# Kernel tuning notes

Hardware: AMD Instinct MI355X
Metric: run time of the kernel (lower is better)

The kernel has to match this reference:

```python
import jax, jax.numpy as jnp
import numpy as np

B, S, D = 4, 2048, 1024
H, K = 16, 64  # n_heads, dim_k (dim_v == dim_k due to __init__ bug)


def setup_inputs() -> dict:
    key = jax.random.key(0)
    ks = jax.random.split(key, 7)
    query = jax.random.normal(ks[0], (B, S, D), dtype=jnp.float32)
    k_in = jax.random.normal(ks[1], (B, S, D), dtype=jnp.float32)
    v_in = jax.random.normal(ks[2], (B, S, D), dtype=jnp.float32)
    scale = 0.02
    Wq = jax.random.normal(ks[3], (H, D, K), dtype=jnp.float32) * scale
    Wk = jax.random.normal(ks[4], (H, D, K), dtype=jnp.float32) * scale
    Wv = jax.random.normal(ks[5], (H, D, K), dtype=jnp.float32) * scale
    Wo = jax.random.normal(ks[6], (H * K, D), dtype=jnp.float32) * scale
    return {"query": query, "key": k_in, "value": v_in,
            "Wq": Wq, "Wk": Wk, "Wv": Wv, "Wo": Wo}


def reference(query, key, value, Wq, Wk, Wv, Wo):
    # Per-head projections, batched over heads: [B,H,S,K]
    q = jnp.einsum('bsd,hdk->bhsk', query, Wq)
    k = jnp.einsum('bsd,hdk->bhsk', key, Wk)
    v = jnp.einsum('bsd,hdk->bhsk', value, Wv)
    scale = jnp.sqrt(jnp.asarray(q.shape[-1], q.dtype))
    scores = jnp.einsum('bhqk,bhmk->bhqm', q, k) / scale  # [B,H,S,S]
    attn = jax.nn.softmax(scores, axis=-1)
    out = jnp.einsum('bhqm,bhmk->bhqk', attn, v)          # [B,H,S,K]
    # Concatenate heads along feature axis: [B,S,H*K]
    concat = out.transpose(0, 2, 1, 3).reshape(out.shape[0], out.shape[2], -1)
    return concat @ Wo  # [B,S,D]
```

## Files before the change

kernel.cpp:

```cpp
#include <hip/hip_runtime.h>


typedef __bf16 bf16;
typedef __bf16 bf16x4 __attribute__((ext_vector_type(4)));
typedef __bf16 bf16x8 __attribute__((ext_vector_type(8)));
typedef float f32x4 __attribute__((ext_vector_type(4)));

#define DEV static __device__ __forceinline__

constexpr int S = 2048;
constexpr int M = 8192;
constexpr int N = 1024;
constexpr int KD = 1024;

constexpr size_t PROJ_BYTES = (size_t)M * N * 2;
constexpr size_t OFF_Q  = 0;
constexpr size_t OFF_K  = PROJ_BYTES;
constexpr size_t OFF_VT = 2 * PROJ_BYTES;
constexpr size_t OFF_AO = 3 * PROJ_BYTES;
constexpr size_t OFF_WQ = 4 * PROJ_BYTES;
constexpr size_t WB     = (size_t)KD * N * 2;
constexpr size_t OFF_WK = OFF_WQ + WB;
constexpr size_t OFF_WV = OFF_WQ + 2 * WB;
constexpr size_t OFF_WO = OFF_WQ + 3 * WB;

DEV f32x4 mfma16(bf16x8 a, bf16x8 b, f32x4 c) {
  return __builtin_amdgcn_mfma_f32_16x16x32_bf16(a, b, c, 0, 0, 0);
}

DEV void gload16(const void* g, void* l) {
  __builtin_amdgcn_global_load_lds(
      (const __attribute__((address_space(1))) void*)g,
      (__attribute__((address_space(3))) void*)l, 16, 0, 0);
}

DEV void cvt16(const float* sp, char* ldsrow, int jx0, int jx1) {
  float4 v0 = *(const float4*)(sp);
  float4 v1 = *(const float4*)(sp + 4);
  float4 v2 = *(const float4*)(sp + 8);
  float4 v3 = *(const float4*)(sp + 12);
  bf16x8 q0, q1;
  q0[0] = (bf16)v0.x; q0[1] = (bf16)v0.y; q0[2] = (bf16)v0.z; q0[3] = (bf16)v0.w;
  q0[4] = (bf16)v1.x; q0[5] = (bf16)v1.y; q0[6] = (bf16)v1.z; q0[7] = (bf16)v1.w;
  q1[0] = (bf16)v2.x; q1[1] = (bf16)v2.y; q1[2] = (bf16)v2.z; q1[3] = (bf16)v2.w;
  q1[4] = (bf16)v3.x; q1[5] = (bf16)v3.y; q1[6] = (bf16)v3.z; q1[7] = (bf16)v3.w;
  *(bf16x8*)(ldsrow + jx0 * 16) = q0;
  *(bf16x8*)(ldsrow + jx1 * 16) = q1;
}

__global__ __launch_bounds__(256) void prep_weights(
    const float* __restrict__ Wq, const float* __restrict__ Wk,
    const float* __restrict__ Wv, const float* __restrict__ Wo,
    bf16* __restrict__ Wqt, bf16* __restrict__ Wkt,
    bf16* __restrict__ Wvt, bf16* __restrict__ Wot) {
  __shared__ bf16 T[64][72];
  const int t = threadIdx.x;
  const int wsel = blockIdx.x >> 8;
  const int tile = blockIdx.x & 255;
  const int ti = tile >> 4, tj = tile & 15;
  const int r = t >> 2, c16 = (t & 3) * 16;

  const float* src;
  if (wsel < 3) {
    const float* W = (wsel == 0) ? Wq : (wsel == 1) ? Wk : Wv;
    src = W + (size_t)ti * 65536 + (size_t)(tj * 64 + r) * 64 + c16;
  } else {
    src = Wo + (size_t)(tj * 64 + r) * 1024 + ti * 64 + c16;
  }
#pragma unroll
  for (int i = 0; i < 16; i += 4) {
    float4 v = *(const float4*)(src + i);
    T[r][c16 + i + 0] = (bf16)v.x;
    T[r][c16 + i + 1] = (bf16)v.y;
    T[r][c16 + i + 2] = (bf16)v.z;
    T[r][c16 + i + 3] = (bf16)v.w;
  }
  __syncthreads();
  bf16x8 o0, o1;
#pragma unroll
  for (int i = 0; i < 8; ++i) o0[i] = T[c16 + i][r];
#pragma unroll
  for (int i = 0; i < 8; ++i) o1[i] = T[c16 + 8 + i][r];
  bf16* dst;
  if (wsel < 3) {
    bf16* O = (wsel == 0) ? Wqt : (wsel == 1) ? Wkt : Wvt;
    dst = O + (size_t)(ti * 64 + r) * 1024 + tj * 64 + c16;
  } else {
    dst = Wot + (size_t)(ti * 64 + r) * 1024 + tj * 64 + c16;
  }
  *(bf16x8*)(dst) = o0;
  *(bf16x8*)(dst + 8) = o1;
}

template <int AF32, int BF32, int OMODE>
__global__ __launch_bounds__(256) void gemm_k(const void* __restrict__ Aptr,
                                              const void* __restrict__ Bptr,
                                              void* __restrict__ Outp) {
  __shared__ bf16 Al[128 * 32];
  __shared__ bf16 Bl[128 * 32];
  const int t = threadIdx.x;
  const int lane = t & 63, wid = t >> 6;
  const int g = lane >> 4, c = lane & 15;
  const int wr = wid >> 1, wc = wid & 1;
  int bx, by;
  if constexpr (OMODE == 1) { bx = blockIdx.x & 63; by = blockIdx.x >> 6; }
  else                      { by = blockIdx.x & 63; bx = blockIdx.x >> 6; }
  const int m0 = by * 128, n0 = bx * 128;

  const int p0 = t, p1 = t + 256;
  const int r0 = p0 >> 2, j0 = (p0 & 3) ^ (r0 & 3);
  const int r1 = p1 >> 2, j1 = (p1 & 3) ^ (r1 & 3);
  char* adst0 = (char*)Al + (size_t)(wid * 64) * 16;
  char* adst1 = (char*)Al + (size_t)(256 + wid * 64) * 16;
  char* bdst0 = (char*)Bl + (size_t)(wid * 64) * 16;
  char* bdst1 = (char*)Bl + (size_t)(256 + wid * 64) * 16;
  const int mS = t >> 1, hS = t & 1;
  const int jS0 = (hS * 2 + 0) ^ (mS & 3);
  const int jS1 = (hS * 2 + 1) ^ (mS & 3);

  const float* Af = (const float*)Aptr;
  const bf16*  Ab = (const bf16*)Aptr;
  const float* Bf = (const float*)Bptr;
  const bf16*  Bb = (const bf16*)Bptr;

  f32x4 acc[4][4];
#pragma unroll
  for (int i = 0; i < 4; ++i)
#pragma unroll
    for (int j = 0; j < 4; ++j) acc[i][j] = f32x4{0.f, 0.f, 0.f, 0.f};

  for (int kt = 0; kt < KD / 32; ++kt) {
    const int k0 = kt * 32;
    if constexpr (AF32) {
      cvt16(Af + (size_t)(m0 + mS) * KD + hS * 16 + k0, (char*)Al + mS * 64,
            jS0, jS1);
    } else {
      gload16(Ab + (size_t)(m0 + r0) * KD + j0 * 8 + k0, adst0);
      gload16(Ab + (size_t)(m0 + r1) * KD + j1 * 8 + k0, adst1);
    }
    if constexpr (BF32) {
      cvt16(Bf + (size_t)(n0 + mS) * KD + hS * 16 + k0, (char*)Bl + mS * 64,
            jS0, jS1);
    } else {
      gload16(Bb + (size_t)(n0 + r0) * KD + j0 * 8 + k0, bdst0);
      gload16(Bb + (size_t)(n0 + r1) * KD + j1 * 8 + k0, bdst1);
    }
    __syncthreads();
    bf16x8 af[4], bfv[4];
#pragma unroll
    for (int mi = 0; mi < 4; ++mi) {
      const int m = wr * 64 + mi * 16 + c;
      af[mi] = *(const bf16x8*)((const char*)Al + m * 64 + ((g ^ (m & 3)) * 16));
    }
#pragma unroll
    for (int ni = 0; ni < 4; ++ni) {
      const int n = wc * 64 + ni * 16 + c;
      bfv[ni] = *(const bf16x8*)((const char*)Bl + n * 64 + ((g ^ (n & 3)) * 16));
    }
#pragma unroll
    for (int mi = 0; mi < 4; ++mi)
#pragma unroll
      for (int ni = 0; ni < 4; ++ni)
        acc[mi][ni] = mfma16(af[mi], bfv[ni], acc[mi][ni]);
    __syncthreads();
  }

#pragma unroll
  for (int mi = 0; mi < 4; ++mi) {
#pragma unroll
    for (int ni = 0; ni < 4; ++ni) {
#pragma unroll
      for (int r = 0; r < 4; ++r) {
        const int m = m0 + wr * 64 + mi * 16 + 4 * g + r;
        const int n = n0 + wc * 64 + ni * 16 + c;
        const float v = acc[mi][ni][r];
        if constexpr (OMODE == 2) {
          ((float*)Outp)[(size_t)m * N + n] = v;
        } else if constexpr (OMODE == 0) {
          const int b = m >> 11, s = m & 2047, h = n >> 6, kk = n & 63;
          ((bf16*)Outp)[((size_t)(b * 16 + h) * 2048 + s) * 64 + kk] = (bf16)v;
        } else {
          const int h = m >> 6, kk = m & 63, b = n >> 11, s = n & 2047;
          ((bf16*)Outp)[((size_t)(b * 16 + h) * 64 + kk) * 2048 + s] = (bf16)v;
        }
      }
    }
  }
}

__global__ __launch_bounds__(256) void attn_k(const bf16* __restrict__ Q,
                                              const bf16* __restrict__ Kg,
                                              const bf16* __restrict__ Vg,
                                              bf16* __restrict__ AO) {
  __shared__ bf16 KT[64 * 64];
  __shared__ bf16 VTl[64 * 64];
  __shared__ bf16 P[4][16][40];
  const int t = threadIdx.x, lane = t & 63, w = t >> 6;
  const int g = lane >> 4, c = lane & 15;
  const int bh = blockIdx.x & 63, qblk = blockIdx.x >> 6;
  const int q0 = qblk * 128 + w * 32;
  const bf16* qp = Q + (size_t)bh * S * 64;
  const bf16* kp = Kg + (size_t)bh * S * 64;
  const bf16* vp = Vg + (size_t)bh * 64 * S;

  bf16x8 qf[2][2];
#pragma unroll
  for (int qt = 0; qt < 2; ++qt)
#pragma unroll
    for (int dh = 0; dh < 2; ++dh)
      qf[qt][dh] =
          *(const bf16x8*)(qp + (size_t)(q0 + qt * 16 + c) * 64 + dh * 32 + g * 8);

  int srow[4], sj[4];
#pragma unroll
  for (int k2 = 0; k2 < 4; ++k2) {
    const int pr = (t + 256 * k2) & 511;
    srow[k2] = pr >> 3;
    sj[k2] = (pr & 7) ^ (srow[k2] & 7);
  }
  bf16* dst0 = KT + (size_t)(w * 64) * 8;
  bf16* dst1 = KT + (size_t)(256 + w * 64) * 8;
  bf16* dst2 = VTl + (size_t)(w * 64) * 8;
  bf16* dst3 = VTl + (size_t)(256 + w * 64) * 8;

  f32x4 ao[2][4];
#pragma unroll
  for (int i = 0; i < 2; ++i)
#pragma unroll
    for (int j = 0; j < 4; ++j) ao[i][j] = f32x4{0.f, 0.f, 0.f, 0.f};
  float mr[2] = {0.f, 0.f};
  float lr[2] = {0.f, 0.f};
  constexpr float SC = 0.18033688011112042f;

  for (int kv0 = 0; kv0 < S; kv0 += 64) {
    gload16(kp + (size_t)(kv0 + srow[0]) * 64 + sj[0] * 8, dst0);
    gload16(kp + (size_t)(kv0 + srow[1]) * 64 + sj[1] * 8, dst1);
    gload16(vp + (size_t)srow[2] * 2048 + kv0 + sj[2] * 8, dst2);
    gload16(vp + (size_t)srow[3] * 2048 + kv0 + sj[3] * 8, dst3);
    __syncthreads();

    f32x4 st[2][4];
#pragma unroll
    for (int i = 0; i < 2; ++i)
#pragma unroll
      for (int j = 0; j < 4; ++j) st[i][j] = f32x4{0.f, 0.f, 0.f, 0.f};
#pragma unroll
    for (int dh = 0; dh < 2; ++dh) {
      bf16x8 kf[4];
#pragma unroll
      for (int sub = 0; sub < 4; ++sub) {
        const int row = sub * 16 + c;
        const int ch = (dh * 4 + g) ^ (row & 7);
        kf[sub] = *(const bf16x8*)(KT + row * 64 + ch * 8);
      }
      __builtin_amdgcn_s_setprio(1);
#pragma unroll
      for (int sub = 0; sub < 4; ++sub) {
        st[0][sub] = mfma16(kf[sub], qf[0][dh], st[0][sub]);
        st[1][sub] = mfma16(kf[sub], qf[1][dh], st[1][sub]);
      }
      __builtin_amdgcn_s_setprio(0);
    }
    bf16x8 vf[4][2];
#pragma unroll
    for (int dt = 0; dt < 4; ++dt) {
      const int row = dt * 16 + c;
#pragma unroll
      for (int s2 = 0; s2 < 2; ++s2) {
        const int ch = (s2 * 4 + g) ^ (row & 7);
        vf[dt][s2] = *(const bf16x8*)(VTl + row * 64 + ch * 8);
      }
    }
#pragma unroll
    for (int qt = 0; qt < 2; ++qt) {
      float rm = st[qt][0][0];
#pragma unroll
      for (int sub = 0; sub < 4; ++sub)
#pragma unroll
        for (int r = 0; r < 4; ++r) rm = fmaxf(rm, st[qt][sub][r]);
      rm = fmaxf(rm, __shfl_xor(rm, 16));
      rm = fmaxf(rm, __shfl_xor(rm, 32));
      const float pm = rm * SC;
      if (!__all(pm - mr[qt] <= 8.0f)) {
        const float mn = fmaxf(mr[qt], pm);
        const float corr = __builtin_amdgcn_exp2f(mr[qt] - mn);
        mr[qt] = mn;
        lr[qt] *= corr;
        float cor[4];
#pragma unroll
        for (int r = 0; r < 4; ++r)
          cor[r] = __shfl(corr, (lane & 48) + 4 * g + r);
#pragma unroll
        for (int dt = 0; dt < 4; ++dt)
#pragma unroll
          for (int r = 0; r < 4; ++r) ao[qt][dt][r] *= cor[r];
      }
      float p[16];
      float sum = 0.f;
#pragma unroll
      for (int sub = 0; sub < 4; ++sub)
#pragma unroll
        for (int r = 0; r < 4; ++r) {
          const float e = __builtin_amdgcn_exp2f(
              __builtin_fmaf(st[qt][sub][r], SC, -mr[qt]));
          p[sub * 4 + r] = e;
          sum += e;
        }
      sum += __shfl_xor(sum, 16);
      sum += __shfl_xor(sum, 32);
      lr[qt] += sum;
#pragma unroll
      for (int hh = 0; hh < 2; ++hh) {
#pragma unroll
        for (int sw = 0; sw < 2; ++sw) {
          bf16x4 t4;
#pragma unroll
          for (int r = 0; r < 4; ++r) t4[r] = (bf16)p[(2 * hh + sw) * 4 + r];
          *(bf16x4*)(&P[w][c][sw * 16 + 4 * g]) = t4;
        }
        const bf16x8 pa = *(const bf16x8*)(&P[w][c][g * 8]);
        __builtin_amdgcn_s_setprio(1);
#pragma unroll
        for (int dt = 0; dt < 4; ++dt)
          ao[qt][dt] = mfma16(pa, vf[dt][hh], ao[qt][dt]);
        __builtin_amdgcn_s_setprio(0);
      }
    }
    __syncthreads();
  }

  const int b = bh >> 4, h = bh & 15;
#pragma unroll
  for (int qt = 0; qt < 2; ++qt) {
    const float iv = 1.0f / lr[qt];
    float linv[4];
#pragma unroll
    for (int r = 0; r < 4; ++r) linv[r] = __shfl(iv, (lane & 48) + 4 * g + r);
#pragma unroll
    for (int dt = 0; dt < 4; ++dt)
#pragma unroll
      for (int r = 0; r < 4; ++r) {
        const int srow = q0 + qt * 16 + 4 * g + r;
        AO[((size_t)(b * 2048 + srow)) * 1024 + h * 64 + dt * 16 + c] =
            (bf16)(ao[qt][dt][r] * linv[r]);
      }
  }
}

extern "C" void kernel_launch(void* const* d_in, const int* in_sizes, int n_in,
                              void* d_out, int out_size, void* d_ws,
                              size_t ws_size, hipStream_t stream) {
  (void)in_sizes; (void)n_in; (void)out_size; (void)ws_size;
  const float* query = (const float*)d_in[0];
  const float* key   = (const float*)d_in[1];
  const float* value = (const float*)d_in[2];
  const float* Wq    = (const float*)d_in[3];
  const float* Wk    = (const float*)d_in[4];
  const float* Wv    = (const float*)d_in[5];
  const float* Wo    = (const float*)d_in[6];

  char* ws = (char*)d_ws;
  bf16* qb  = (bf16*)(ws + OFF_Q);
  bf16* kb  = (bf16*)(ws + OFF_K);
  bf16* vtb = (bf16*)(ws + OFF_VT);
  bf16* aob = (bf16*)(ws + OFF_AO);
  bf16* wqt = (bf16*)(ws + OFF_WQ);
  bf16* wkt = (bf16*)(ws + OFF_WK);
  bf16* wvt = (bf16*)(ws + OFF_WV);
  bf16* wot = (bf16*)(ws + OFF_WO);

  prep_weights<<<1024, 256, 0, stream>>>(Wq, Wk, Wv, Wo, wqt, wkt, wvt, wot);
  gemm_k<1, 0, 0><<<512, 256, 0, stream>>>(query, wqt, qb);
  gemm_k<1, 0, 0><<<512, 256, 0, stream>>>(key, wkt, kb);
  gemm_k<0, 1, 1><<<512, 256, 0, stream>>>(wvt, value, vtb);
  attn_k<<<1024, 256, 0, stream>>>(qb, kb, vtb, aob);
  gemm_k<0, 0, 2><<<512, 256, 0, stream>>>(aob, wot, (float*)d_out);
}
```

Measured before the change: 417.8 us.

## Double-buffer GEMM and attention LDS, pre-convert inputs, enlarge attention query tile

Input activations are now converted from fp32 to bf16 in a separate elementwise kernel, so every GEMM streams bf16 through async global-to-LDS loads. Both the GEMM and the attention kernel double-buffer their LDS tiles, prefetching the next K-step while computing the current one and removing one barrier per iteration. The attention kernel processes 64 query rows per wave instead of 32, halving the grid and reusing each K/V tile across more queries, and it writes the full 64-wide P tile at once. The costs are three extra conversion passes over the inputs, higher register pressure in attention, and doubled shared memory.

```diff
diff --git a/kernel.cpp b/kernel.cpp
--- a/kernel.cpp
+++ b/kernel.cpp
@@ -13,12 +13,12 @@
 constexpr int N = 1024;
 constexpr int KD = 1024;
 
-constexpr size_t PROJ_BYTES = (size_t)M * N * 2;
-constexpr size_t OFF_Q  = 0;
-constexpr size_t OFF_K  = PROJ_BYTES;
-constexpr size_t OFF_VT = 2 * PROJ_BYTES;
-constexpr size_t OFF_AO = 3 * PROJ_BYTES;
-constexpr size_t OFF_WQ = 4 * PROJ_BYTES;
+constexpr size_t RGN = (size_t)M * N * 2;
+constexpr size_t OFF_QB = 0;
+constexpr size_t OFF_KB = RGN;
+constexpr size_t OFF_VT = 2 * RGN;
+constexpr size_t OFF_XB = 3 * RGN;
+constexpr size_t OFF_WQ = 4 * RGN;
 constexpr size_t WB     = (size_t)KD * N * 2;
 constexpr size_t OFF_WK = OFF_WQ + WB;
 constexpr size_t OFF_WV = OFF_WQ + 2 * WB;
@@ -34,18 +34,18 @@
       (__attribute__((address_space(3))) void*)l, 16, 0, 0);
 }
 
-DEV void cvt16(const float* sp, char* ldsrow, int jx0, int jx1) {
-  float4 v0 = *(const float4*)(sp);
-  float4 v1 = *(const float4*)(sp + 4);
-  float4 v2 = *(const float4*)(sp + 8);
-  float4 v3 = *(const float4*)(sp + 12);
-  bf16x8 q0, q1;
-  q0[0] = (bf16)v0.x; q0[1] = (bf16)v0.y; q0[2] = (bf16)v0.z; q0[3] = (bf16)v0.w;
-  q0[4] = (bf16)v1.x; q0[5] = (bf16)v1.y; q0[6] = (bf16)v1.z; q0[7] = (bf16)v1.w;
-  q1[0] = (bf16)v2.x; q1[1] = (bf16)v2.y; q1[2] = (bf16)v2.z; q1[3] = (bf16)v2.w;
-  q1[4] = (bf16)v3.x; q1[5] = (bf16)v3.y; q1[6] = (bf16)v3.z; q1[7] = (bf16)v3.w;
-  *(bf16x8*)(ldsrow + jx0 * 16) = q0;
-  *(bf16x8*)(ldsrow + jx1 * 16) = q1;
+__global__ __launch_bounds__(256) void prep_in(const float* __restrict__ X,
+                                               bf16* __restrict__ Y) {
+  const int i0 = blockIdx.x * 256 + threadIdx.x;
+  const int stride = gridDim.x * 256;
+  for (int i = i0; i < (1 << 20); i += stride) {
+    float4 a = ((const float4*)X)[2 * i];
+    float4 b = ((const float4*)X)[2 * i + 1];
+    bf16x8 o;
+    o[0] = (bf16)a.x; o[1] = (bf16)a.y; o[2] = (bf16)a.z; o[3] = (bf16)a.w;
+    o[4] = (bf16)b.x; o[5] = (bf16)b.y; o[6] = (bf16)b.z; o[7] = (bf16)b.w;
+    ((bf16x8*)Y)[i] = o;
+  }
 }
 
 __global__ __launch_bounds__(256) void prep_weights(
@@ -92,12 +92,12 @@
   *(bf16x8*)(dst + 8) = o1;
 }
 
-template <int AF32, int BF32, int OMODE>
-__global__ __launch_bounds__(256) void gemm_k(const void* __restrict__ Aptr,
-                                              const void* __restrict__ Bptr,
+template <int OMODE>
+__global__ __launch_bounds__(256) void gemm_k(const bf16* __restrict__ A,
+                                              const bf16* __restrict__ Bt,
                                               void* __restrict__ Outp) {
-  __shared__ bf16 Al[128 * 32];
-  __shared__ bf16 Bl[128 * 32];
+  __shared__ bf16 Al[2][128 * 32];
+  __shared__ bf16 Bl[2][128 * 32];
   const int t = threadIdx.x;
   const int lane = t & 63, wid = t >> 6;
   const int g = lane >> 4, c = lane & 15;
@@ -110,18 +110,10 @@
   const int p0 = t, p1 = t + 256;
   const int r0 = p0 >> 2, j0 = (p0 & 3) ^ (r0 & 3);
   const int r1 = p1 >> 2, j1 = (p1 & 3) ^ (r1 & 3);
-  char* adst0 = (char*)Al + (size_t)(wid * 64) * 16;
-  char* adst1 = (char*)Al + (size_t)(256 + wid * 64) * 16;
-  char* bdst0 = (char*)Bl + (size_t)(wid * 64) * 16;
-  char* bdst1 = (char*)Bl + (size_t)(256 + wid * 64) * 16;
-  const int mS = t >> 1, hS = t & 1;
-  const int jS0 = (hS * 2 + 0) ^ (mS & 3);
-  const int jS1 = (hS * 2 + 1) ^ (mS & 3);
-
-  const float* Af = (const float*)Aptr;
-  const bf16*  Ab = (const bf16*)Aptr;
-  const float* Bf = (const float*)Bptr;
-  const bf16*  Bb = (const bf16*)Bptr;
+  const bf16* as0 = A + (size_t)(m0 + r0) * KD + j0 * 8;
+  const bf16* as1 = A + (size_t)(m0 + r1) * KD + j1 * 8;
+  const bf16* bs0 = Bt + (size_t)(n0 + r0) * KD + j0 * 8;
+  const bf16* bs1 = Bt + (size_t)(n0 + r1) * KD + j1 * 8;
 
   f32x4 acc[4][4];
 #pragma unroll
@@ -129,33 +121,32 @@
 #pragma unroll
     for (int j = 0; j < 4; ++j) acc[i][j] = f32x4{0.f, 0.f, 0.f, 0.f};
 
+#define STAGE_G(buf, k0)                                                     \
+  do {                                                                       \
+    gload16(as0 + (k0), (char*)Al[buf] + (size_t)(wid * 64) * 16);           \
+    gload16(as1 + (k0), (char*)Al[buf] + (size_t)(256 + wid * 64) * 16);     \
+    gload16(bs0 + (k0), (char*)Bl[buf] + (size_t)(wid * 64) * 16);           \
+    gload16(bs1 + (k0), (char*)Bl[buf] + (size_t)(256 + wid * 64) * 16);     \
+  } while (0)
+
+  STAGE_G(0, 0);
+  __syncthreads();
+
   for (int kt = 0; kt < KD / 32; ++kt) {
-    const int k0 = kt * 32;
-    if constexpr (AF32) {
-      cvt16(Af + (size_t)(m0 + mS) * KD + hS * 16 + k0, (char*)Al + mS * 64,
-            jS0, jS1);
-    } else {
-      gload16(Ab + (size_t)(m0 + r0) * KD + j0 * 8 + k0, adst0);
-      gload16(Ab + (size_t)(m0 + r1) * KD + j1 * 8 + k0, adst1);
-    }
-    if constexpr (BF32) {
-      cvt16(Bf + (size_t)(n0 + mS) * KD + hS * 16 + k0, (char*)Bl + mS * 64,
-            jS0, jS1);
-    } else {
-      gload16(Bb + (size_t)(n0 + r0) * KD + j0 * 8 + k0, bdst0);
-      gload16(Bb + (size_t)(n0 + r1) * KD + j1 * 8 + k0, bdst1);
-    }
-    __syncthreads();
+    const int cur = kt & 1;
+    if (kt < KD / 32 - 1) STAGE_G(cur ^ 1, (kt + 1) * 32);
     bf16x8 af[4], bfv[4];
 #pragma unroll
     for (int mi = 0; mi < 4; ++mi) {
       const int m = wr * 64 + mi * 16 + c;
-      af[mi] = *(const bf16x8*)((const char*)Al + m * 64 + ((g ^ (m & 3)) * 16));
+      af[mi] = *(const bf16x8*)((const char*)Al[cur] + m * 64 +
+                                ((g ^ (m & 3)) * 16));
     }
 #pragma unroll
     for (int ni = 0; ni < 4; ++ni) {
       const int n = wc * 64 + ni * 16 + c;
-      bfv[ni] = *(const bf16x8*)((const char*)Bl + n * 64 + ((g ^ (n & 3)) * 16));
+      bfv[ni] = *(const bf16x8*)((const char*)Bl[cur] + n * 64 +
+                                 ((g ^ (n & 3)) * 16));
     }
 #pragma unroll
     for (int mi = 0; mi < 4; ++mi)
@@ -164,6 +155,7 @@
         acc[mi][ni] = mfma16(af[mi], bfv[ni], acc[mi][ni]);
     __syncthreads();
   }
+#undef STAGE_G
 
 #pragma unroll
   for (int mi = 0; mi < 4; ++mi) {
@@ -188,28 +180,28 @@
   }
 }
 
-__global__ __launch_bounds__(256) void attn_k(const bf16* __restrict__ Q,
-                                              const bf16* __restrict__ Kg,
-                                              const bf16* __restrict__ Vg,
-                                              bf16* __restrict__ AO) {
-  __shared__ bf16 KT[64 * 64];
-  __shared__ bf16 VTl[64 * 64];
-  __shared__ bf16 P[4][16][40];
+__global__ __launch_bounds__(256, 2) void attn_k(const bf16* __restrict__ Q,
+                                                 const bf16* __restrict__ Kg,
+                                                 const bf16* __restrict__ Vg,
+                                                 bf16* __restrict__ AO) {
+  __shared__ bf16 KT[2][64 * 64];
+  __shared__ bf16 VT[2][64 * 64];
+  __shared__ bf16 P[4][16][72];
   const int t = threadIdx.x, lane = t & 63, w = t >> 6;
   const int g = lane >> 4, c = lane & 15;
   const int bh = blockIdx.x & 63, qblk = blockIdx.x >> 6;
-  const int q0 = qblk * 128 + w * 32;
+  const int q0 = qblk * 256 + w * 64;
   const bf16* qp = Q + (size_t)bh * S * 64;
   const bf16* kp = Kg + (size_t)bh * S * 64;
   const bf16* vp = Vg + (size_t)bh * 64 * S;
 
-  bf16x8 qf[2][2];
-#pragma unroll
-  for (int qt = 0; qt < 2; ++qt)
+  bf16x8 qf[4][2];
+#pragma unroll
+  for (int qt = 0; qt < 4; ++qt)
 #pragma unroll
     for (int dh = 0; dh < 2; ++dh)
-      qf[qt][dh] =
-          *(const bf16x8*)(qp + (size_t)(q0 + qt * 16 + c) * 64 + dh * 32 + g * 8);
+      qf[qt][dh] = *(const bf16x8*)(qp + (size_t)(q0 + qt * 16 + c) * 64 +
+                                    dh * 32 + g * 8);
 
   int srow[4], sj[4];
 #pragma unroll
@@ -218,30 +210,38 @@
     srow[k2] = pr >> 3;
     sj[k2] = (pr & 7) ^ (srow[k2] & 7);
   }
-  bf16* dst0 = KT + (size_t)(w * 64) * 8;
-  bf16* dst1 = KT + (size_t)(256 + w * 64) * 8;
-  bf16* dst2 = VTl + (size_t)(w * 64) * 8;
-  bf16* dst3 = VTl + (size_t)(256 + w * 64) * 8;
-
-  f32x4 ao[2][4];
-#pragma unroll
-  for (int i = 0; i < 2; ++i)
+
+#define STAGE_A(buf, kv0)                                                     \
+  do {                                                                        \
+    gload16(kp + (size_t)((kv0) + srow[0]) * 64 + sj[0] * 8,                  \
+            KT[buf] + w * 512);                                               \
+    gload16(kp + (size_t)((kv0) + srow[1]) * 64 + sj[1] * 8,                  \
+            KT[buf] + 2048 + w * 512);                                        \
+    gload16(vp + (size_t)srow[2] * 2048 + (kv0) + sj[2] * 8,                  \
+            VT[buf] + w * 512);                                               \
+    gload16(vp + (size_t)srow[3] * 2048 + (kv0) + sj[3] * 8,                  \
+            VT[buf] + 2048 + w * 512);                                        \
+  } while (0)
+
+  f32x4 ao[4][4];
+#pragma unroll
+  for (int i = 0; i < 4; ++i)
 #pragma unroll
     for (int j = 0; j < 4; ++j) ao[i][j] = f32x4{0.f, 0.f, 0.f, 0.f};
-  float mr[2] = {0.f, 0.f};
-  float lr[2] = {0.f, 0.f};
+  float mr[4] = {0.f, 0.f, 0.f, 0.f};
+  float lr[4] = {0.f, 0.f, 0.f, 0.f};
   constexpr float SC = 0.18033688011112042f;
 
-  for (int kv0 = 0; kv0 < S; kv0 += 64) {
-    gload16(kp + (size_t)(kv0 + srow[0]) * 64 + sj[0] * 8, dst0);
-    gload16(kp + (size_t)(kv0 + srow[1]) * 64 + sj[1] * 8, dst1);
-    gload16(vp + (size_t)srow[2] * 2048 + kv0 + sj[2] * 8, dst2);
-    gload16(vp + (size_t)srow[3] * 2048 + kv0 + sj[3] * 8, dst3);
-    __syncthreads();
-
-    f32x4 st[2][4];
-#pragma unroll
-    for (int i = 0; i < 2; ++i)
+  STAGE_A(0, 0);
+  __syncthreads();
+
+  for (int it = 0; it < 32; ++it) {
+    const int cur = it & 1;
+    if (it < 31) STAGE_A(cur ^ 1, (it + 1) * 64);
+
+    f32x4 st[4][4];
+#pragma unroll
+    for (int i = 0; i < 4; ++i)
 #pragma unroll
       for (int j = 0; j < 4; ++j) st[i][j] = f32x4{0.f, 0.f, 0.f, 0.f};
 #pragma unroll
@@ -250,15 +250,15 @@
 #pragma unroll
       for (int sub = 0; sub < 4; ++sub) {
         const int row = sub * 16 + c;
-        const int ch = (dh * 4 + g) ^ (row & 7);
-        kf[sub] = *(const bf16x8*)(KT + row * 64 + ch * 8);
+        const int ch = (dh * 4 + g) ^ (c & 7);
+        kf[sub] = *(const bf16x8*)(&KT[cur][row * 64 + ch * 8]);
       }
       __builtin_amdgcn_s_setprio(1);
 #pragma unroll
-      for (int sub = 0; sub < 4; ++sub) {
-        st[0][sub] = mfma16(kf[sub], qf[0][dh], st[0][sub]);
-        st[1][sub] = mfma16(kf[sub], qf[1][dh], st[1][sub]);
-      }
+      for (int sub = 0; sub < 4; ++sub)
+#pragma unroll
+        for (int qt = 0; qt < 4; ++qt)
+          st[qt][sub] = mfma16(kf[sub], qf[qt][dh], st[qt][sub]);
       __builtin_amdgcn_s_setprio(0);
     }
     bf16x8 vf[4][2];
@@ -267,12 +267,12 @@
       const int row = dt * 16 + c;
 #pragma unroll
       for (int s2 = 0; s2 < 2; ++s2) {
-        const int ch = (s2 * 4 + g) ^ (row & 7);
-        vf[dt][s2] = *(const bf16x8*)(VTl + row * 64 + ch * 8);
-      }
-    }
-#pragma unroll
-    for (int qt = 0; qt < 2; ++qt) {
+        const int ch = (s2 * 4 + g) ^ (c & 7);
+        vf[dt][s2] = *(const bf16x8*)(&VT[cur][row * 64 + ch * 8]);
+      }
+    }
+#pragma unroll
+    for (int qt = 0; qt < 4; ++qt) {
       float rm = st[qt][0][0];
 #pragma unroll
       for (int sub = 0; sub < 4; ++sub)
@@ -295,7 +295,6 @@
 #pragma unroll
           for (int r = 0; r < 4; ++r) ao[qt][dt][r] *= cor[r];
       }
-      float p[16];
       float sum = 0.f;
 #pragma unroll
       for (int sub = 0; sub < 4; ++sub)
@@ -303,35 +302,36 @@
         for (int r = 0; r < 4; ++r) {
           const float e = __builtin_amdgcn_exp2f(
               __builtin_fmaf(st[qt][sub][r], SC, -mr[qt]));
-          p[sub * 4 + r] = e;
+          st[qt][sub][r] = e;
           sum += e;
         }
       sum += __shfl_xor(sum, 16);
       sum += __shfl_xor(sum, 32);
       lr[qt] += sum;
 #pragma unroll
-      for (int hh = 0; hh < 2; ++hh) {
-#pragma unroll
-        for (int sw = 0; sw < 2; ++sw) {
-          bf16x4 t4;
-#pragma unroll
-          for (int r = 0; r < 4; ++r) t4[r] = (bf16)p[(2 * hh + sw) * 4 + r];
-          *(bf16x4*)(&P[w][c][sw * 16 + 4 * g]) = t4;
-        }
-        const bf16x8 pa = *(const bf16x8*)(&P[w][c][g * 8]);
-        __builtin_amdgcn_s_setprio(1);
-#pragma unroll
-        for (int dt = 0; dt < 4; ++dt)
-          ao[qt][dt] = mfma16(pa, vf[dt][hh], ao[qt][dt]);
-        __builtin_amdgcn_s_setprio(0);
-      }
+      for (int sub = 0; sub < 4; ++sub) {
+        bf16x4 t4;
+#pragma unroll
+        for (int r = 0; r < 4; ++r) t4[r] = (bf16)st[qt][sub][r];
+        *(bf16x4*)(&P[w][c][sub * 16 + 4 * g]) = t4;
+      }
+      const bf16x8 pa0 = *(const bf16x8*)(&P[w][c][8 * g]);
+      const bf16x8 pa1 = *(const bf16x8*)(&P[w][c][32 + 8 * g]);
+      __builtin_amdgcn_s_setprio(1);
+#pragma unroll
+      for (int dt = 0; dt < 4; ++dt) {
+        ao[qt][dt] = mfma16(pa0, vf[dt][0], ao[qt][dt]);
+        ao[qt][dt] = mfma16(pa1, vf[dt][1], ao[qt][dt]);
+      }
+      __builtin_amdgcn_s_setprio(0);
     }
     __syncthreads();
   }
+#undef STAGE_A
 
   const int b = bh >> 4, h = bh & 15;
 #pragma unroll
-  for (int qt = 0; qt < 2; ++qt) {
+  for (int qt = 0; qt < 4; ++qt) {
     const float iv = 1.0f / lr[qt];
     float linv[4];
 #pragma unroll
@@ -360,19 +360,22 @@
   const float* Wo    = (const float*)d_in[6];
 
   char* ws = (char*)d_ws;
-  bf16* qb  = (bf16*)(ws + OFF_Q);
-  bf16* kb  = (bf16*)(ws + OFF_K);
+  bf16* qb  = (bf16*)(ws + OFF_QB);
+  bf16* kb  = (bf16*)(ws + OFF_KB);
   bf16* vtb = (bf16*)(ws + OFF_VT);
-  bf16* aob = (bf16*)(ws + OFF_AO);
+  bf16* xb  = (bf16*)(ws + OFF_XB);
   bf16* wqt = (bf16*)(ws + OFF_WQ);
   bf16* wkt = (bf16*)(ws + OFF_WK);
   bf16* wvt = (bf16*)(ws + OFF_WV);
   bf16* wot = (bf16*)(ws + OFF_WO);
 
   prep_weights<<<1024, 256, 0, stream>>>(Wq, Wk, Wv, Wo, wqt, wkt, wvt, wot);
-  gemm_k<1, 0, 0><<<512, 256, 0, stream>>>(query, wqt, qb);
-  gemm_k<1, 0, 0><<<512, 256, 0, stream>>>(key, wkt, kb);
-  gemm_k<0, 1, 1><<<512, 256, 0, stream>>>(wvt, value, vtb);
-  attn_k<<<1024, 256, 0, stream>>>(qb, kb, vtb, aob);
-  gemm_k<0, 0, 2><<<512, 256, 0, stream>>>(aob, wot, (float*)d_out);
-}
+  prep_in<<<2048, 256, 0, stream>>>(query, xb);
+  gemm_k<0><<<512, 256, 0, stream>>>(xb, wqt, qb);
+  prep_in<<<2048, 256, 0, stream>>>(key, xb);
+  gemm_k<0><<<512, 256, 0, stream>>>(xb, wkt, kb);
+  prep_in<<<2048, 256, 0, stream>>>(value, xb);
+  gemm_k<1><<<512, 256, 0, stream>>>(wvt, xb, vtb);
+  attn_k<<<512, 256, 0, stream>>>(qb, kb, vtb, xb);
+  gemm_k<2><<<512, 256, 0, stream>>>(xb, wot, (float*)d_out);
+}
```

Measured after the change: 376.2 us. 1.11x faster.
